# Optimization experiments

Measured on AMD Instinct MI355X. Metric: run time of the kernel, lower is better.

Reference implementation:

```python
import jax, jax.numpy as jnp
import numpy as np

BETA = 0.25
EPS = 1e-12  # torch F.normalize eps


def _l2_normalize(x, axis):
    n = jnp.linalg.norm(x, axis=axis, keepdims=True)
    return x / jnp.maximum(n, EPS)


def setup_inputs() -> dict:
    key = jax.random.key(0)
    k1, k2 = jax.random.split(key)
    z = jax.random.normal(k1, (16, 256, 64, 64), dtype=jnp.float32)
    K = 1024
    embedding = jax.random.uniform(k2, (K, 256), dtype=jnp.float32,
                                   minval=-1.0 / K, maxval=1.0 / K)
    return {"z": z, "embedding": embedding}


def reference(z, embedding):
    # Faithful to torch source: normalize over the LAST axis of [B,C,H,W] (the W axis)
    zn = _l2_normalize(z, axis=-1)
    zp = jnp.transpose(zn, (0, 2, 3, 1))            # [B,H,W,C]
    B, H, W, C = zp.shape
    zf = zp.reshape(-1, C)                           # [N, C], N = B*H*W
    wn = _l2_normalize(embedding, axis=-1)           # normalized codebook for distances
    # d[n,k] = ||zf_n||^2 + ||wn_k||^2 - 2 zf_n . wn_k
    d = (jnp.sum(zf * zf, axis=1, keepdims=True)
         + jnp.sum(wn * wn, axis=1)
         - 2.0 * jnp.einsum('nc,kc->nk', zf, wn))
    idx = jnp.argmin(d, axis=1)                      # [N] int
    # gather uses the UN-normalized embedding (as in torch source)
    z_q = embedding[idx].reshape(B, H, W, C)
    # training-mode commitment loss + straight-through estimator
    loss = (BETA * jnp.mean((jax.lax.stop_gradient(z_q) - zp) ** 2)
            + jnp.mean((z_q - jax.lax.stop_gradient(zp)) ** 2))
    z_q = zp + jax.lax.stop_gradient(z_q - zp)
    z_q = jnp.transpose(z_q, (0, 3, 1, 2))           # back to [B,C,H,W]
    return z_q, idx, loss
```

## Files before the change

### kernel.cpp

```cpp
#include <hip/hip_runtime.h>

#define NN 65536
#define KK 1024
#define TFLAG_FIX 2098u

typedef __bf16 bf16x8 __attribute__((ext_vector_type(8)));
typedef float f32x16 __attribute__((ext_vector_type(16)));

__device__ __forceinline__ unsigned short f2bf(float x){
  unsigned u = __float_as_uint(x);
  u += 0x7FFFu + ((u >> 16) & 1u);
  return (unsigned short)(u >> 16);
}
__device__ __forceinline__ float bf2f(unsigned short h){
  return __uint_as_float(((unsigned)h) << 16);
}
__device__ __forceinline__ void dma16(const uint4* g, uint4* l){
  __builtin_amdgcn_global_load_lds(
      (const __attribute__((address_space(1))) void*)g,
      (__attribute__((address_space(3))) void*)l, 16, 0, 0);
}
__device__ __forceinline__ unsigned long long shfl_xor_u64(unsigned long long v, int m){
  unsigned lo = (unsigned)__shfl_xor((int)(unsigned)v, m, 64);
  unsigned hi = (unsigned)__shfl_xor((int)(unsigned)(v >> 32), m, 64);
  return ((unsigned long long)hi << 32) | lo;
}
union U4S8 { uint4 v; unsigned short u[8]; };


__global__ __launch_bounds__(64) void kern_prep(const float* __restrict__ emb,
    float* __restrict__ wnT, uint4* __restrict__ wnh4,
    float* __restrict__ wnn, float* __restrict__ wnn4)
{
  const int k = blockIdx.x, t = threadIdx.x;
  float4 v = ((const float4*)emb)[k*64 + t];
  float ss = fmaf(v.x, v.x, fmaf(v.y, v.y, fmaf(v.z, v.z, v.w * v.w)));
  #pragma unroll
  for (int m = 32; m > 0; m >>= 1) ss += __shfl_xor(ss, m, 64);
  float d = fmaxf(sqrtf(ss), 1e-12f);
  float w0 = v.x / d, w1 = v.y / d, w2 = v.z / d, w3 = v.w / d;
  wnT[(size_t)(4*t+0)*1024 + k] = w0;
  wnT[(size_t)(4*t+1)*1024 + k] = w1;
  wnT[(size_t)(4*t+2)*1024 + k] = w2;
  wnT[(size_t)(4*t+3)*1024 + k] = w3;
  unsigned short* base = (unsigned short*)wnh4;
  size_t o = ((size_t)(k >> 5) * 1024 + (size_t)(t >> 1) * 32 + (k & 31)) * 8 + (t & 1) * 4;
  base[o+0] = f2bf(w0); base[o+1] = f2bf(w1); base[o+2] = f2bf(w2); base[o+3] = f2bf(w3);
  float s2 = fmaf(w0, w0, fmaf(w1, w1, fmaf(w2, w2, w3 * w3)));
  #pragma unroll
  for (int m = 32; m > 0; m >>= 1) s2 += __shfl_xor(s2, m, 64);
  if (t == 0){ wnn[k] = s2; wnn4[k] = 4.0f - s2; }
}

__global__ __launch_bounds__(256) void kern_znorm(const float* __restrict__ z,
    uint4* __restrict__ zfh4, uint4* __restrict__ zfl4)
{
  __shared__ float tile[64][65];
  __shared__ float sinv[64];
  const int t = threadIdx.x;
  const int ct = blockIdx.x & 3;
  const int bh = blockIdx.x >> 2;
  const int c0 = ct * 64, q0 = ct * 8;
  const int cl = t >> 2, q = t & 3;
  const float4* zr = (const float4*)(z + ((size_t)(bh >> 6) * 256 + c0 + cl) * 4096
                                       + (size_t)(bh & 63) * 64);
  #pragma unroll
  for (int i = 0; i < 4; i++){
    float4 v = zr[q + 4*i];
    int w = (q + 4*i) * 4;
    tile[cl][w] = v.x; tile[cl][w+1] = v.y; tile[cl][w+2] = v.z; tile[cl][w+3] = v.w;
  }
  __syncthreads();
  if (t < 64){
    float ss = 0.f;
    #pragma unroll
    for (int w = 0; w < 64; w++){ float x = tile[t][w]; ss = fmaf(x, x, ss); }
    sinv[t] = 1.0f / fmaxf(sqrtf(ss), 1e-12f);
  }
  __syncthreads();
  #pragma unroll
  for (int j = 0; j < 2; j++){
    int p = t + 256 * j;
    int tI = p >> 8, rem = p & 255;
    int qq = rem >> 5, colI = rem & 31;
    int w = tI * 32 + colI;
    U4S8 hh, ll;
    #pragma unroll
    for (int e = 0; e < 8; e++){
      int c = qq * 8 + e;
      float v = tile[c][w] * sinv[c];
      hh.u[e] = f2bf(v);
      ll.u[e] = f2bf(v - bf2f(hh.u[e]));
    }
    size_t o = (size_t)(bh * 2 + tI) * 1024 + (size_t)(q0 + qq) * 32 + colI;
    zfh4[o] = hh.v;
    zfl4[o] = ll.v;
  }
}

__global__ __launch_bounds__(256, 2) void kern_gemm(
    const uint4* __restrict__ zA, const uint4* __restrict__ wB,
    const float* __restrict__ wnn4, uint2* __restrict__ pairs)
{
  __shared__ uint4 sB[2][1024];
  const int t = threadIdx.x;
  const int wv = t >> 6;
  const int lane = t & 63;
  const int col = lane & 31;
  const int half = lane >> 5;
  const int hb = blockIdx.x & 1;
  const int cb = hb * 512;
  const int rowBase = (blockIdx.x >> 1) * 256 + wv * 64;
  const int T0 = rowBase >> 5;

  bf16x8 a0[16], a1[16];
  {
    const uint4* r0 = zA + (size_t)T0 * 1024;
    const uint4* r1 = zA + (size_t)(T0 + 1) * 1024;
    const uint4* g0 = wB + (size_t)(cb >> 5) * 1024;
    dma16(g0 + (wv*4+0)*64 + lane, &sB[0][(wv*4+0)*64 + lane]);
    dma16(g0 + (wv*4+1)*64 + lane, &sB[0][(wv*4+1)*64 + lane]);
    dma16(g0 + (wv*4+2)*64 + lane, &sB[0][(wv*4+2)*64 + lane]);
    dma16(g0 + (wv*4+3)*64 + lane, &sB[0][(wv*4+3)*64 + lane]);
    #pragma unroll
    for (int s = 0; s < 16; s++){
      a0[s] = __builtin_bit_cast(bf16x8, r0[(2*s + half)*32 + col]);
      a1[s] = __builtin_bit_cast(bf16x8, r1[(2*s + half)*32 + col]);
    }
  }
  unsigned b1k[2][16], b2k[2][16];
  #pragma unroll
  for (int r = 0; r < 16; r++){
    b1k[0][r] = 0u; b1k[1][r] = 0u; b2k[0][r] = 0u; b2k[1][r] = 0u;
  }
  const int kinvBase = 1023 - cb - col;
  __syncthreads();

  for (int kt = 0; kt < 16; kt++){
    if (kt < 15){
      const uint4* gn = wB + (size_t)((cb >> 5) + kt + 1) * 1024;
      uint4* ld = &sB[(kt + 1) & 1][0];
      dma16(gn + (wv*4+0)*64 + lane, ld + (wv*4+0)*64 + lane);
      dma16(gn + (wv*4+1)*64 + lane, ld + (wv*4+1)*64 + lane);
      dma16(gn + (wv*4+2)*64 + lane, ld + (wv*4+2)*64 + lane);
      dma16(gn + (wv*4+3)*64 + lane, ld + (wv*4+3)*64 + lane);
    }
    const float c4k = wnn4[cb + kt*32 + col];
    const uint4* bp = &sB[kt & 1][half * 32 + col];
    f32x16 acc0, acc1;
    #pragma unroll
    for (int i = 0; i < 16; i++){ acc0[i] = 0.0f; acc1[i] = 0.0f; }
    #pragma unroll
    for (int s = 0; s < 16; s++){
      bf16x8 bs = __builtin_bit_cast(bf16x8, bp[s * 64]);
      acc0 = __builtin_amdgcn_mfma_f32_32x32x16_bf16(a0[s], bs, acc0, 0, 0, 0);
      acc1 = __builtin_amdgcn_mfma_f32_32x32x16_bf16(a1[s], bs, acc1, 0, 0, 0);
    }
    const unsigned kinv = (unsigned)(kinvBase - kt * 32);
    #pragma unroll
    for (int r = 0; r < 16; r++){
      float s0 = fmaf(2.0f, acc0[r], c4k);
      unsigned u0 = ((unsigned)(s0 * 524288.0f) << 10) | kinv;
      b2k[0][r] = max(b2k[0][r], min(b1k[0][r], u0));
      b1k[0][r] = max(b1k[0][r], u0);
      float s1 = fmaf(2.0f, acc1[r], c4k);
      unsigned u1 = ((unsigned)(s1 * 524288.0f) << 10) | kinv;
      b2k[1][r] = max(b2k[1][r], min(b1k[1][r], u1));
      b1k[1][r] = max(b1k[1][r], u1);
    }
    __syncthreads();
  }
  #pragma unroll
  for (int m = 1; m < 32; m <<= 1){
    #pragma unroll
    for (int ti = 0; ti < 2; ti++){
      #pragma unroll
      for (int r = 0; r < 16; r++){
        unsigned o1 = (unsigned)__shfl_xor((int)b1k[ti][r], m, 64);
        unsigned o2 = (unsigned)__shfl_xor((int)b2k[ti][r], m, 64);
        b2k[ti][r] = max(max(b2k[ti][r], o2), min(b1k[ti][r], o1));
        b1k[ti][r] = max(b1k[ti][r], o1);
      }
    }
  }
  if (col == 0){
    #pragma unroll
    for (int ti = 0; ti < 2; ti++){
      #pragma unroll
      for (int r = 0; r < 16; r++){
        int rowD = (r & 3) + 8 * (r >> 2) + 4 * half;
        int n = rowBase + ti * 32 + rowD;
        pairs[(size_t)n * 2 + hb] = make_uint2(b1k[ti][r], b2k[ti][r]);
      }
    }
  }
}

__global__ __launch_bounds__(256) void kern_merge(
    const uint2* __restrict__ pairs, int* __restrict__ idx_i, float* __restrict__ idx_f,
    int* __restrict__ flag_list, unsigned int* __restrict__ flag_count)
{
  const int n = blockIdx.x * 256 + threadIdx.x;
  uint2 p0 = pairs[(size_t)n * 2];
  uint2 p1 = pairs[(size_t)n * 2 + 1];
  unsigned B1 = max(p0.x, p1.x);
  unsigned B2 = max(max(p0.y, p1.y), min(p0.x, p1.x));
  int idx = 1023 - (int)(B1 & 1023u);
  idx_i[n] = idx;
  idx_f[n] = (float)idx;
  bool f = ((B1 >> 10) - (B2 >> 10)) < TFLAG_FIX;
  unsigned long long m = __ballot(f);
  if (m){
    int lane = threadIdx.x & 63;
    int leader = __ffsll((unsigned long long)m) - 1;
    unsigned base = 0;
    if (lane == leader) base = atomicAdd(flag_count, (unsigned)__popcll(m));
    base = (unsigned)__shfl((int)base, leader, 64);
    if (f){
      int off = __popcll(m & ((1ull << lane) - 1ull));
      flag_list[base + off] = n;
    }
  }
}

__global__ __launch_bounds__(256) void kern_rescue(
    const uint4* __restrict__ zfh4, const uint4* __restrict__ zfl4,
    const float* __restrict__ wnT, const float* __restrict__ wnn,
    const int* __restrict__ flag_list, const unsigned int* __restrict__ flag_count,
    unsigned long long* __restrict__ keys)
{
  __shared__ float sz[16][256];
  __shared__ unsigned long long sred[4][16];
  __shared__ int srow[16];
  const int t = threadIdx.x;
  const int lane = t & 63, wvi = t >> 6;
  const int cnt = (int)*flag_count;
  const int hb = blockIdx.x & 1;
  const int bb = blockIdx.x >> 1;
  if (bb * 16 >= cnt) return;
  const int k0 = hb * 512 + t * 2;
  const float wq0 = wnn[k0+0], wq1 = wnn[k0+1];
  const float2* wt2 = (const float2*)wnT;
  const size_t ko2 = (size_t)(k0 >> 1);

  for (int base = bb * 16; base < cnt; base += (gridDim.x >> 1) * 16){
    const int nr = min(16, cnt - base);
    __syncthreads();
    if (t < 16) srow[t] = flag_list[base + min(t, nr - 1)];
    __syncthreads();
    #pragma unroll
    for (int j = 0; j < 2; j++){
      int p = t + j * 256;
      int r = p >> 5, q = p & 31;
      int n = srow[r];
      size_t o = (size_t)(n >> 5) * 1024 + (size_t)q * 32 + (n & 31);
      U4S8 h, l; h.v = zfh4[o]; l.v = zfl4[o];
      #pragma unroll
      for (int e = 0; e < 8; e++) sz[r][q*8+e] = bf2f(h.u[e]) + bf2f(l.u[e]);
    }
    __syncthreads();

    float acc[2][16];
    #pragma unroll
    for (int j = 0; j < 2; j++)
      #pragma unroll
      for (int r = 0; r < 16; r++) acc[j][r] = 0.0f;
    for (int c4 = 0; c4 < 64; c4++){
      float2 cv0 = wt2[(size_t)(4*c4+0)*512 + ko2];
      float2 cv1 = wt2[(size_t)(4*c4+1)*512 + ko2];
      float2 cv2 = wt2[(size_t)(4*c4+2)*512 + ko2];
      float2 cv3 = wt2[(size_t)(4*c4+3)*512 + ko2];
      #pragma unroll
      for (int r = 0; r < 16; r++){
        float4 s = ((const float4*)sz[r])[c4];
        acc[0][r] = fmaf(s.x, cv0.x, acc[0][r]);
        acc[0][r] = fmaf(s.y, cv1.x, acc[0][r]);
        acc[0][r] = fmaf(s.z, cv2.x, acc[0][r]);
        acc[0][r] = fmaf(s.w, cv3.x, acc[0][r]);
        acc[1][r] = fmaf(s.x, cv0.y, acc[1][r]);
        acc[1][r] = fmaf(s.y, cv1.y, acc[1][r]);
        acc[1][r] = fmaf(s.z, cv2.y, acc[1][r]);
        acc[1][r] = fmaf(s.w, cv3.y, acc[1][r]);
      }
    }
    #pragma unroll
    for (int r = 0; r < 16; r++){
      float s0 = fmaf(-2.0f, acc[0][r], wq0);
      float s1 = fmaf(-2.0f, acc[1][r], wq1);
      float bv = s0; int bi = k0;
      if (s1 < bv){ bv = s1; bi = k0 + 1; }
      unsigned u = __float_as_uint(bv);
      u = (u & 0x80000000u) ? ~u : (u | 0x80000000u);
      unsigned long long key = ((unsigned long long)u << 10) | (unsigned)bi;
      #pragma unroll
      for (int m = 1; m < 64; m <<= 1){
        unsigned long long o = shfl_xor_u64(key, m);
        if (o < key) key = o;
      }
      if (lane == 0) sred[wvi][r] = key;
    }
    __syncthreads();
    if (t < nr){
      unsigned long long ka = sred[0][t] < sred[1][t] ? sred[0][t] : sred[1][t];
      unsigned long long kb = sred[2][t] < sred[3][t] ? sred[2][t] : sred[3][t];
      unsigned long long kf = ka < kb ? ka : kb;
      keys[(size_t)srow[t] * 2 + hb] = kf;
    }
  }
}

__global__ __launch_bounds__(256) void kern_rescue_fin(
    const unsigned long long* __restrict__ keys, const int* __restrict__ flag_list,
    const unsigned int* __restrict__ flag_count,
    int* __restrict__ idx_i, float* __restrict__ idx_f)
{
  const int cnt = (int)*flag_count;
  for (int i = blockIdx.x * 256 + threadIdx.x; i < cnt; i += gridDim.x * 256){
    int n = flag_list[i];
    unsigned long long ka = keys[(size_t)n * 2];
    unsigned long long kb = keys[(size_t)n * 2 + 1];
    unsigned long long kf = ka < kb ? ka : kb;
    int fi = (int)(kf & 1023ull);
    idx_i[n] = fi;
    idx_f[n] = (float)fi;
  }
}

__global__ __launch_bounds__(256) void kern_gather(
    const float* __restrict__ z, const float* __restrict__ emb,
    const int* __restrict__ idx_i, float* __restrict__ out,
    float* __restrict__ loss_acc)
{
  __shared__ float zq[64][65];
  __shared__ int sidx[64];
  __shared__ float swsum[4];
  const int t = threadIdx.x;
  const int ct = blockIdx.x & 3;
  const int bh = blockIdx.x >> 2;
  const int c0 = ct * 64;
  if (t < 64) sidx[t] = idx_i[bh*64 + t];

  const int r = t >> 2, w0 = (t & 3) * 16;
  const float4* zr = (const float4*)(z + ((size_t)(bh >> 6) * 256 + c0 + r) * 4096
                                       + (size_t)(bh & 63) * 64 + w0);
  float4 tz0 = zr[0], tz1 = zr[1], tz2 = zr[2], tz3 = zr[3];
  __syncthreads();

  {
    const int ch4 = (t & 15) * 4, wrow = t >> 4;
    #pragma unroll
    for (int it = 0; it < 4; it++){
      int w = wrow + 16*it;
      float4 qv = *(const float4*)(emb + (size_t)sidx[w] * 256 + c0 + ch4);
      zq[ch4+0][w] = qv.x; zq[ch4+1][w] = qv.y;
      zq[ch4+2][w] = qv.z; zq[ch4+3][w] = qv.w;
    }
  }
  float ss = 0.f;
  ss = fmaf(tz0.x, tz0.x, ss); ss = fmaf(tz0.y, tz0.y, ss);
  ss = fmaf(tz0.z, tz0.z, ss); ss = fmaf(tz0.w, tz0.w, ss);
  ss = fmaf(tz1.x, tz1.x, ss); ss = fmaf(tz1.y, tz1.y, ss);
  ss = fmaf(tz1.z, tz1.z, ss); ss = fmaf(tz1.w, tz1.w, ss);
  ss = fmaf(tz2.x, tz2.x, ss); ss = fmaf(tz2.y, tz2.y, ss);
  ss = fmaf(tz2.z, tz2.z, ss); ss = fmaf(tz2.w, tz2.w, ss);
  ss = fmaf(tz3.x, tz3.x, ss); ss = fmaf(tz3.y, tz3.y, ss);
  ss = fmaf(tz3.z, tz3.z, ss); ss = fmaf(tz3.w, tz3.w, ss);
  ss += __shfl_xor(ss, 1, 64);
  ss += __shfl_xor(ss, 2, 64);
  const float inv = 1.0f / fmaxf(sqrtf(ss), 1e-12f);
  __syncthreads();

  float lsum = 0.f;
  float* op = out + ((size_t)(bh >> 6) * 256 + c0 + r) * 4096
                  + (size_t)(bh & 63) * 64 + w0;
  #pragma unroll
  for (int i = 0; i < 4; i++){
    float4 tzv = (i == 0) ? tz0 : (i == 1) ? tz1 : (i == 2) ? tz2 : tz3;
    int w = w0 + 4*i;
    float q0 = zq[r][w+0], q1 = zq[r][w+1], q2 = zq[r][w+2], q3 = zq[r][w+3];
    float d0 = q0 - tzv.x * inv;
    float d1 = q1 - tzv.y * inv;
    float d2 = q2 - tzv.z * inv;
    float d3 = q3 - tzv.w * inv;
    lsum = fmaf(d0, d0, lsum); lsum = fmaf(d1, d1, lsum);
    lsum = fmaf(d2, d2, lsum); lsum = fmaf(d3, d3, lsum);
    ((float4*)op)[i] = make_float4(q0, q1, q2, q3);
  }
  #pragma unroll
  for (int m = 32; m > 0; m >>= 1) lsum += __shfl_down(lsum, m, 64);
  if ((t & 63) == 0) swsum[t >> 6] = lsum;
  __syncthreads();
  if (t == 0) atomicAdd(loss_acc, swsum[0] + swsum[1] + swsum[2] + swsum[3]);
}

__global__ void kern_final(const float* __restrict__ loss_acc, float* __restrict__ out_loss){
  if (threadIdx.x == 0 && blockIdx.x == 0)
    out_loss[0] = 1.25f * loss_acc[0] * (1.0f / 16777216.0f);
}

extern "C" void kernel_launch(void* const* d_in, const int* in_sizes, int n_in,
                              void* d_out, int out_size, void* d_ws, size_t ws_size,
                              hipStream_t stream)
{
  const float* z   = (const float*)d_in[0];
  const float* emb = (const float*)d_in[1];
  char* ws = (char*)d_ws;
  unsigned int* flag_count = (unsigned int*)(ws + 0);
  float* loss_acc          = (float*)(ws + 8);
  float* wnn               = (float*)(ws + 1024);
  float* wnn4              = (float*)(ws + 8192);
  float* wnT               = (float*)(ws + 16384);
  uint4* wnh4              = (uint4*)(ws + 1064960);
  int* idx_i               = (int*)(ws + 1589248);
  int* flag_list           = (int*)(ws + 1851392);
  uint2* pairs             = (uint2*)(ws + 2113536);
  unsigned long long* keys = (unsigned long long*)(ws + 2113536);
  uint4* zfh4              = (uint4*)(ws + 3162112);
  uint4* zfl4              = (uint4*)(ws + 36716544);
  float* out_zq   = (float*)d_out;
  float* out_idx  = (float*)d_out + 16777216;
  float* out_loss = (float*)d_out + 16842752;

  hipMemsetAsync(ws, 0, 16, stream);
  kern_prep<<<KK, 64, 0, stream>>>(emb, wnT, wnh4, wnn, wnn4);
  kern_znorm<<<4096, 256, 0, stream>>>(z, zfh4, zfl4);
  kern_gemm<<<512, 256, 0, stream>>>(zfh4, wnh4, wnn4, pairs);
  kern_merge<<<256, 256, 0, stream>>>(pairs, idx_i, out_idx, flag_list, flag_count);
  kern_rescue<<<1024, 256, 0, stream>>>(zfh4, zfl4, wnT, wnn, flag_list, flag_count,
                                        keys);
  kern_rescue_fin<<<64, 256, 0, stream>>>(keys, flag_list, flag_count, idx_i, out_idx);
  kern_gather<<<4096, 256, 0, stream>>>(z, emb, idx_i, out_zq, loss_acc);
  kern_final<<<1, 64, 0, stream>>>(loss_acc, out_loss);
}
```

Baseline: 298.8 us.

## Run rescue and gather concurrently in one launch, then patch changed rows

Merges the rescue GEMM and the gather/loss kernel into a single launch, with the block index choosing the role and a shared-memory union holding each role's buffers. The gather works from the tentative indices, so it can overlap the rescue work instead of waiting for it. A small patch kernel then resolves the rescued indices. For each row whose index changed it rewrites the output row and index and corrects the loss with the difference of squared errors. This removes a launch and a serialization point, in exchange for scattered patch writes and a loss correction whose float rounding differs slightly from computing it directly.

```diff
diff --git a/kernel.cpp b/kernel.cpp
--- a/kernel.cpp
+++ b/kernel.cpp
@@ -223,122 +223,112 @@
   }
 }
 
-__global__ __launch_bounds__(256) void kern_rescue(
+struct RescueSM {
+  float sz[16][256];
+  unsigned long long sred[4][16];
+  int srow[16];
+};
+struct GatherSM {
+  float zq[64][65];
+  int sidx[64];
+  float swsum[4];
+};
+
+__global__ __launch_bounds__(256) void kern_fused(
+    const float* __restrict__ z, const float* __restrict__ emb,
+    const int* __restrict__ idx_i, float* __restrict__ out,
+    float* __restrict__ loss_acc,
     const uint4* __restrict__ zfh4, const uint4* __restrict__ zfl4,
     const float* __restrict__ wnT, const float* __restrict__ wnn,
     const int* __restrict__ flag_list, const unsigned int* __restrict__ flag_count,
     unsigned long long* __restrict__ keys)
 {
-  __shared__ float sz[16][256];
-  __shared__ unsigned long long sred[4][16];
-  __shared__ int srow[16];
+  __shared__ union { RescueSM r; GatherSM g; } sm;
   const int t = threadIdx.x;
-  const int lane = t & 63, wvi = t >> 6;
-  const int cnt = (int)*flag_count;
-  const int hb = blockIdx.x & 1;
-  const int bb = blockIdx.x >> 1;
-  if (bb * 16 >= cnt) return;
-  const int k0 = hb * 512 + t * 2;
-  const float wq0 = wnn[k0+0], wq1 = wnn[k0+1];
-  const float2* wt2 = (const float2*)wnT;
-  const size_t ko2 = (size_t)(k0 >> 1);
-
-  for (int base = bb * 16; base < cnt; base += (gridDim.x >> 1) * 16){
-    const int nr = min(16, cnt - base);
-    __syncthreads();
-    if (t < 16) srow[t] = flag_list[base + min(t, nr - 1)];
-    __syncthreads();
-    #pragma unroll
-    for (int j = 0; j < 2; j++){
-      int p = t + j * 256;
-      int r = p >> 5, q = p & 31;
-      int n = srow[r];
-      size_t o = (size_t)(n >> 5) * 1024 + (size_t)q * 32 + (n & 31);
-      U4S8 h, l; h.v = zfh4[o]; l.v = zfl4[o];
-      #pragma unroll
-      for (int e = 0; e < 8; e++) sz[r][q*8+e] = bf2f(h.u[e]) + bf2f(l.u[e]);
-    }
-    __syncthreads();
-
-    float acc[2][16];
-    #pragma unroll
-    for (int j = 0; j < 2; j++)
-      #pragma unroll
-      for (int r = 0; r < 16; r++) acc[j][r] = 0.0f;
-    for (int c4 = 0; c4 < 64; c4++){
-      float2 cv0 = wt2[(size_t)(4*c4+0)*512 + ko2];
-      float2 cv1 = wt2[(size_t)(4*c4+1)*512 + ko2];
-      float2 cv2 = wt2[(size_t)(4*c4+2)*512 + ko2];
-      float2 cv3 = wt2[(size_t)(4*c4+3)*512 + ko2];
+
+  if (blockIdx.x < 1024){
+    const int lane = t & 63, wvi = t >> 6;
+    const int cnt = (int)*flag_count;
+    const int hb = blockIdx.x & 1;
+    const int bb = blockIdx.x >> 1;
+    if (bb * 16 >= cnt) return;
+    const int k0 = hb * 512 + t * 2;
+    const float wq0 = wnn[k0+0], wq1 = wnn[k0+1];
+    const float2* wt2 = (const float2*)wnT;
+    const size_t ko2 = (size_t)(k0 >> 1);
+
+    for (int base = bb * 16; base < cnt; base += 512 * 16){
+      const int nr = min(16, cnt - base);
+      __syncthreads();
+      if (t < 16) sm.r.srow[t] = flag_list[base + min(t, nr - 1)];
+      __syncthreads();
+      #pragma unroll
+      for (int j = 0; j < 2; j++){
+        int p = t + j * 256;
+        int r = p >> 5, q = p & 31;
+        int n = sm.r.srow[r];
+        size_t o = (size_t)(n >> 5) * 1024 + (size_t)q * 32 + (n & 31);
+        U4S8 h, l; h.v = zfh4[o]; l.v = zfl4[o];
+        #pragma unroll
+        for (int e = 0; e < 8; e++) sm.r.sz[r][q*8+e] = bf2f(h.u[e]) + bf2f(l.u[e]);
+      }
+      __syncthreads();
+
+      float acc[2][16];
+      #pragma unroll
+      for (int j = 0; j < 2; j++)
+        #pragma unroll
+        for (int r = 0; r < 16; r++) acc[j][r] = 0.0f;
+      for (int c4 = 0; c4 < 64; c4++){
+        float2 cv0 = wt2[(size_t)(4*c4+0)*512 + ko2];
+        float2 cv1 = wt2[(size_t)(4*c4+1)*512 + ko2];
+        float2 cv2 = wt2[(size_t)(4*c4+2)*512 + ko2];
+        float2 cv3 = wt2[(size_t)(4*c4+3)*512 + ko2];
+        #pragma unroll
+        for (int r = 0; r < 16; r++){
+          float4 s = ((const float4*)sm.r.sz[r])[c4];
+          acc[0][r] = fmaf(s.x, cv0.x, acc[0][r]);
+          acc[0][r] = fmaf(s.y, cv1.x, acc[0][r]);
+          acc[0][r] = fmaf(s.z, cv2.x, acc[0][r]);
+          acc[0][r] = fmaf(s.w, cv3.x, acc[0][r]);
+          acc[1][r] = fmaf(s.x, cv0.y, acc[1][r]);
+          acc[1][r] = fmaf(s.y, cv1.y, acc[1][r]);
+          acc[1][r] = fmaf(s.z, cv2.y, acc[1][r]);
+          acc[1][r] = fmaf(s.w, cv3.y, acc[1][r]);
+        }
+      }
       #pragma unroll
       for (int r = 0; r < 16; r++){
-        float4 s = ((const float4*)sz[r])[c4];
-        acc[0][r] = fmaf(s.x, cv0.x, acc[0][r]);
-        acc[0][r] = fmaf(s.y, cv1.x, acc[0][r]);
-        acc[0][r] = fmaf(s.z, cv2.x, acc[0][r]);
-        acc[0][r] = fmaf(s.w, cv3.x, acc[0][r]);
-        acc[1][r] = fmaf(s.x, cv0.y, acc[1][r]);
-        acc[1][r] = fmaf(s.y, cv1.y, acc[1][r]);
-        acc[1][r] = fmaf(s.z, cv2.y, acc[1][r]);
-        acc[1][r] = fmaf(s.w, cv3.y, acc[1][r]);
-      }
-    }
-    #pragma unroll
-    for (int r = 0; r < 16; r++){
-      float s0 = fmaf(-2.0f, acc[0][r], wq0);
-      float s1 = fmaf(-2.0f, acc[1][r], wq1);
-      float bv = s0; int bi = k0;
-      if (s1 < bv){ bv = s1; bi = k0 + 1; }
-      unsigned u = __float_as_uint(bv);
-      u = (u & 0x80000000u) ? ~u : (u | 0x80000000u);
-      unsigned long long key = ((unsigned long long)u << 10) | (unsigned)bi;
-      #pragma unroll
-      for (int m = 1; m < 64; m <<= 1){
-        unsigned long long o = shfl_xor_u64(key, m);
-        if (o < key) key = o;
-      }
-      if (lane == 0) sred[wvi][r] = key;
-    }
-    __syncthreads();
-    if (t < nr){
-      unsigned long long ka = sred[0][t] < sred[1][t] ? sred[0][t] : sred[1][t];
-      unsigned long long kb = sred[2][t] < sred[3][t] ? sred[2][t] : sred[3][t];
-      unsigned long long kf = ka < kb ? ka : kb;
-      keys[(size_t)srow[t] * 2 + hb] = kf;
-    }
-  }
-}
-
-__global__ __launch_bounds__(256) void kern_rescue_fin(
-    const unsigned long long* __restrict__ keys, const int* __restrict__ flag_list,
-    const unsigned int* __restrict__ flag_count,
-    int* __restrict__ idx_i, float* __restrict__ idx_f)
-{
-  const int cnt = (int)*flag_count;
-  for (int i = blockIdx.x * 256 + threadIdx.x; i < cnt; i += gridDim.x * 256){
-    int n = flag_list[i];
-    unsigned long long ka = keys[(size_t)n * 2];
-    unsigned long long kb = keys[(size_t)n * 2 + 1];
-    unsigned long long kf = ka < kb ? ka : kb;
-    int fi = (int)(kf & 1023ull);
-    idx_i[n] = fi;
-    idx_f[n] = (float)fi;
-  }
-}
-
-__global__ __launch_bounds__(256) void kern_gather(
-    const float* __restrict__ z, const float* __restrict__ emb,
-    const int* __restrict__ idx_i, float* __restrict__ out,
-    float* __restrict__ loss_acc)
-{
-  __shared__ float zq[64][65];
-  __shared__ int sidx[64];
-  __shared__ float swsum[4];
-  const int t = threadIdx.x;
-  const int ct = blockIdx.x & 3;
-  const int bh = blockIdx.x >> 2;
+        float s0 = fmaf(-2.0f, acc[0][r], wq0);
+        float s1 = fmaf(-2.0f, acc[1][r], wq1);
+        float bv = s0; int bi = k0;
+        if (s1 < bv){ bv = s1; bi = k0 + 1; }
+        unsigned u = __float_as_uint(bv);
+        u = (u & 0x80000000u) ? ~u : (u | 0x80000000u);
+        unsigned long long key = ((unsigned long long)u << 10) | (unsigned)bi;
+        #pragma unroll
+        for (int m = 1; m < 64; m <<= 1){
+          unsigned long long o = shfl_xor_u64(key, m);
+          if (o < key) key = o;
+        }
+        if (lane == 0) sm.r.sred[wvi][r] = key;
+      }
+      __syncthreads();
+      if (t < nr){
+        unsigned long long ka = sm.r.sred[0][t] < sm.r.sred[1][t] ? sm.r.sred[0][t] : sm.r.sred[1][t];
+        unsigned long long kb = sm.r.sred[2][t] < sm.r.sred[3][t] ? sm.r.sred[2][t] : sm.r.sred[3][t];
+        unsigned long long kf = ka < kb ? ka : kb;
+        keys[(size_t)sm.r.srow[t] * 2 + hb] = kf;
+      }
+    }
+    return;
+  }
+
+  const int gb = blockIdx.x - 1024;
+  const int ct = gb & 3;
+  const int bh = gb >> 2;
   const int c0 = ct * 64;
-  if (t < 64) sidx[t] = idx_i[bh*64 + t];
+  if (t < 64) sm.g.sidx[t] = idx_i[bh*64 + t];
 
   const int r = t >> 2, w0 = (t & 3) * 16;
   const float4* zr = (const float4*)(z + ((size_t)(bh >> 6) * 256 + c0 + r) * 4096
@@ -351,9 +341,9 @@
     #pragma unroll
     for (int it = 0; it < 4; it++){
       int w = wrow + 16*it;
-      float4 qv = *(const float4*)(emb + (size_t)sidx[w] * 256 + c0 + ch4);
-      zq[ch4+0][w] = qv.x; zq[ch4+1][w] = qv.y;
-      zq[ch4+2][w] = qv.z; zq[ch4+3][w] = qv.w;
+      float4 qv = *(const float4*)(emb + (size_t)sm.g.sidx[w] * 256 + c0 + ch4);
+      sm.g.zq[ch4+0][w] = qv.x; sm.g.zq[ch4+1][w] = qv.y;
+      sm.g.zq[ch4+2][w] = qv.z; sm.g.zq[ch4+3][w] = qv.w;
     }
   }
   float ss = 0.f;
@@ -377,7 +367,8 @@
   for (int i = 0; i < 4; i++){
     float4 tzv = (i == 0) ? tz0 : (i == 1) ? tz1 : (i == 2) ? tz2 : tz3;
     int w = w0 + 4*i;
-    float q0 = zq[r][w+0], q1 = zq[r][w+1], q2 = zq[r][w+2], q3 = zq[r][w+3];
+    float q0 = sm.g.zq[r][w+0], q1 = sm.g.zq[r][w+1];
+    float q2 = sm.g.zq[r][w+2], q3 = sm.g.zq[r][w+3];
     float d0 = q0 - tzv.x * inv;
     float d1 = q1 - tzv.y * inv;
     float d2 = q2 - tzv.z * inv;
@@ -388,9 +379,57 @@
   }
   #pragma unroll
   for (int m = 32; m > 0; m >>= 1) lsum += __shfl_down(lsum, m, 64);
-  if ((t & 63) == 0) swsum[t >> 6] = lsum;
-  __syncthreads();
-  if (t == 0) atomicAdd(loss_acc, swsum[0] + swsum[1] + swsum[2] + swsum[3]);
+  if ((t & 63) == 0) sm.g.swsum[t >> 6] = lsum;
+  __syncthreads();
+  if (t == 0) atomicAdd(loss_acc, sm.g.swsum[0] + sm.g.swsum[1] + sm.g.swsum[2] + sm.g.swsum[3]);
+}
+
+__global__ __launch_bounds__(256) void kern_patch(
+    const uint4* __restrict__ zfh4, const uint4* __restrict__ zfl4,
+    const float* __restrict__ emb, const unsigned long long* __restrict__ keys,
+    const int* __restrict__ flag_list, const unsigned int* __restrict__ flag_count,
+    const int* __restrict__ idx_i, float* __restrict__ out_idx,
+    float* __restrict__ out, float* __restrict__ loss_acc)
+{
+  const int cnt = (int)*flag_count;
+  const int wvi = threadIdx.x >> 6, lane = threadIdx.x & 63;
+  float dsum = 0.f;
+  for (int i = blockIdx.x * 4 + wvi; i < cnt; i += gridDim.x * 4){
+    const int n = flag_list[i];
+    unsigned long long ka = keys[(size_t)n * 2];
+    unsigned long long kb = keys[(size_t)n * 2 + 1];
+    unsigned long long kf = ka < kb ? ka : kb;
+    const int fi = (int)(kf & 1023ull);
+    const int old = idx_i[n];
+    if (fi == old) continue;
+    if (lane == 0) out_idx[n] = (float)fi;
+    if (lane < 32){
+      size_t o = (size_t)(n >> 5) * 1024 + (size_t)lane * 32 + (n & 31);
+      U4S8 h, l; h.v = zfh4[o]; l.v = zfl4[o];
+      const float4* eo4 = (const float4*)(emb + (size_t)old * 256 + lane * 8);
+      const float4* en4 = (const float4*)(emb + (size_t)fi  * 256 + lane * 8);
+      float4 eo0 = eo4[0], eo1 = eo4[1];
+      float4 en0 = en4[0], en1 = en4[1];
+      float zp[8];
+      #pragma unroll
+      for (int e = 0; e < 8; e++) zp[e] = bf2f(h.u[e]) + bf2f(l.u[e]);
+      float dn, do_;
+      dn = en0.x - zp[0]; do_ = eo0.x - zp[0]; dsum += dn*dn - do_*do_;
+      dn = en0.y - zp[1]; do_ = eo0.y - zp[1]; dsum += dn*dn - do_*do_;
+      dn = en0.z - zp[2]; do_ = eo0.z - zp[2]; dsum += dn*dn - do_*do_;
+      dn = en0.w - zp[3]; do_ = eo0.w - zp[3]; dsum += dn*dn - do_*do_;
+      dn = en1.x - zp[4]; do_ = eo1.x - zp[4]; dsum += dn*dn - do_*do_;
+      dn = en1.y - zp[5]; do_ = eo1.y - zp[5]; dsum += dn*dn - do_*do_;
+      dn = en1.z - zp[6]; do_ = eo1.z - zp[6]; dsum += dn*dn - do_*do_;
+      dn = en1.w - zp[7]; do_ = eo1.w - zp[7]; dsum += dn*dn - do_*do_;
+      float* ob = out + ((size_t)(n >> 12) * 256 + lane * 8) * 4096 + (n & 4095);
+      ob[0*4096] = en0.x; ob[1*4096] = en0.y; ob[2*4096] = en0.z; ob[3*4096] = en0.w;
+      ob[4*4096] = en1.x; ob[5*4096] = en1.y; ob[6*4096] = en1.z; ob[7*4096] = en1.w;
+    }
+  }
+  #pragma unroll
+  for (int m = 1; m < 32; m <<= 1) dsum += __shfl_xor(dsum, m, 64);
+  if (lane == 0 && dsum != 0.f) atomicAdd(loss_acc, dsum);
 }
 
 __global__ void kern_final(const float* __restrict__ loss_acc, float* __restrict__ out_loss){
@@ -426,9 +465,10 @@
   kern_znorm<<<4096, 256, 0, stream>>>(z, zfh4, zfl4);
   kern_gemm<<<512, 256, 0, stream>>>(zfh4, wnh4, wnn4, pairs);
   kern_merge<<<256, 256, 0, stream>>>(pairs, idx_i, out_idx, flag_list, flag_count);
-  kern_rescue<<<1024, 256, 0, stream>>>(zfh4, zfl4, wnT, wnn, flag_list, flag_count,
-                                        keys);
-  kern_rescue_fin<<<64, 256, 0, stream>>>(keys, flag_list, flag_count, idx_i, out_idx);
-  kern_gather<<<4096, 256, 0, stream>>>(z, emb, idx_i, out_zq, loss_acc);
+  kern_fused<<<5120, 256, 0, stream>>>(z, emb, idx_i, out_zq, loss_acc,
+                                       zfh4, zfl4, wnT, wnn, flag_list, flag_count,
+                                       keys);
+  kern_patch<<<128, 256, 0, stream>>>(zfh4, zfl4, emb, keys, flag_list, flag_count,
+                                      idx_i, out_idx, out_zq, loss_acc);
   kern_final<<<1, 64, 0, stream>>>(loss_acc, out_loss);
 }
```

Measured after the change: 272.3 us. -8.9%, faster.
